# Kernel optimization log

Measured on AMD Instinct MI355X. Metric: run time of the kernel, lower is better.

## Reference

```python
import jax, jax.numpy as jnp
import numpy as np
from jax import lax

# dims
B, N, F = 128, 65536, 512


def setup_inputs() -> dict:
    key = jax.random.key(0)
    k1, k2 = jax.random.split(key)
    x = jax.random.normal(k1, (B, N), dtype=jnp.float32)          # dry audio
    logits = jax.random.normal(k2, (B, F, 5), dtype=jnp.float32)  # [bs, n_frames, 5]
    return {"x": x, "logits": logits}


def linear_interpolate_dim1(v, n_out):
    # v: [B, n_in, C] -> [B, n_out, C], linear interp with align_corners=True
    n_in = v.shape[1]
    pos = jnp.arange(n_out, dtype=jnp.float32) * ((n_in - 1) / (n_out - 1))
    i0 = jnp.clip(jnp.floor(pos).astype(jnp.int32), 0, n_in - 2)
    frac = (pos - i0.astype(jnp.float32))[None, :, None]
    return v[:, i0, :] * (1.0 - frac) + v[:, i0 + 1, :] * frac


def logits_to_a_coeff_triangle(a_logits):
    # stability-triangle parameterization: |a2| < 1 and |a1| < 1 + a2
    a1 = 2.0 * jnp.tanh(a_logits[..., 0])
    a1_abs = jnp.abs(a1)
    a2 = 0.5 * ((2.0 - a1_abs) * jnp.tanh(a_logits[..., 1]) + a1_abs)
    return jnp.stack([a1, a2], axis=-1)  # [B, F, 2]


def sample_wise_lpc2(x, a):
    # y[n] = x[n] - a1[n]*y[n-1] - a2[n]*y[n-2];  x: [B,N], a: [B,N,2]
    def step(carry, inp):
        y1, y2 = carry
        xn, a1, a2 = inp
        y = xn - a1 * y1 - a2 * y2
        return (y, y1), y
    z = jnp.zeros(x.shape[0], dtype=x.dtype)
    xs = (x.T, a[:, :, 0].T, a[:, :, 1].T)  # time-major
    _, ys = lax.scan(step, (z, z), xs)
    return ys.T


def time_varying_fir(x, b):
    # y[n] = b0[n]*x[n] + b1[n]*x[n-1] + b2[n]*x[n-2];  b: [B,N,3]
    xp = jnp.pad(x, ((0, 0), (2, 0)))
    return b[:, :, 0] * xp[:, 2:] + b[:, :, 1] * xp[:, 1:-1] + b[:, :, 2] * xp[:, :-2]


def reference(x, logits):
    n_samples = x.shape[1]
    # interp_logits=False: map a-logits to coeffs at frame rate, then interpolate
    a_coeff = logits_to_a_coeff_triangle(logits[..., :2])          # [B, F, 2]
    b_coeff = logits[..., 2:]                                      # [B, F, 3]
    a_coeff = linear_interpolate_dim1(a_coeff, n_samples)          # [B, N, 2]
    b_coeff = linear_interpolate_dim1(b_coeff, n_samples)          # [B, N, 3]
    y_a = sample_wise_lpc2(x, a_coeff)
    y_ab = time_varying_fir(y_a, b_coeff)
    return y_ab
```

## Files before the change

kernel.cpp:

```cpp
#include <hip/hip_runtime.h>
#include <hip/hip_bf16.h>

#define B_   128
#define N_   65536
#define F_   512
#define CS   64
#define CPR  (N_ / CS)
#define TPB  128
#define BPR  (CPR / TPB)
#define NBLK (B_ * BPR)
#define BLK_SAMP (TPB * CS)
#define KPOS ((float)(511.0 / 65535.0))
#define INVK ((float)(65535.0 / 511.0))
#define STRIDE 68
#define MAGIC 0x5A17F00Du

__device__ __forceinline__ float tanh_map1(float l) { return 2.0f * tanhf(l); }

__device__ __forceinline__ void chunk_geom(int n0, float& pos0, int& I, int& kc) {
    pos0 = (float)n0 * KPOS;
    I = min((int)pos0, F_ - 2);
    int k = (int)ceilf(((float)(I + 1) - pos0) * INVK);
    k = max(0, min(k, CS));
    if (k > 0 && (int)((float)(n0 + k - 1) * KPOS) > I) --k;
    else if (k < CS && (int)((float)(n0 + k) * KPOS) <= I) ++k;
    if ((int)pos0 > F_ - 2) k = CS;
    if (I == F_ - 2) {
        if ((float)n0 * KPOS >= (float)(F_ - 1)) k = CS;
    }
    kc = k;
}

__global__ __launch_bounds__(TPB, 2) void fused_lb(const float* __restrict__ x,
                                                   const float* __restrict__ logits,
                                                   float* __restrict__ agg,
                                                   unsigned int* __restrict__ flags,
                                                   float* __restrict__ out) {
    __shared__ __align__(16) float buf[TPB][STRIDE];
    __shared__ float sc[6][TPB];
    __shared__ float sbs[2];
    int tid = threadIdx.x;
    int gid = blockIdx.x;
    int gchunk0 = gid * TPB;

    const float4* xg = (const float4*)x + (size_t)gchunk0 * (CS / 4);
    #pragma unroll
    for (int it = 0; it < BLK_SAMP / 4 / TPB; ++it) {
        int i4 = it * TPB + tid;
        float4 v = xg[i4];
        *(float4*)&buf[i4 >> 4][(i4 & 15) * 4] = v;
    }
    __syncthreads();

    int t = gchunk0 + tid;
    int b = t >> 10;
    int c = t & (CPR - 1);
    int n0 = c * CS;

    float pos0; int I, kc;
    chunk_geom(n0, pos0, I, kc);
    int I2 = min(I + 2, F_ - 1);
    const float* Lg = logits + (size_t)b * F_ * 5;
    float a1A = tanh_map1(Lg[I * 5 + 0]);
    float a1B = tanh_map1(Lg[(I + 1) * 5 + 0]);
    float a1C = tanh_map1(Lg[I2 * 5 + 0]);
    float t1A = tanhf(Lg[I * 5 + 1]);
    float t1B = tanhf(Lg[(I + 1) * 5 + 1]);
    float t1C = tanhf(Lg[I2 * 5 + 1]);
    float a2A = 0.5f * ((2.0f - fabsf(a1A)) * t1A + fabsf(a1A));
    float a2B = 0.5f * ((2.0f - fabsf(a1B)) * t1B + fabsf(a1B));
    float a2C = 0.5f * ((2.0f - fabsf(a1C)) * t1C + fabsf(a1C));

    float If = (float)I;
    float C1  = fmaf(pos0 - If,        a1B - a1A, a1A), D1  = KPOS * (a1B - a1A);
    float C1b = fmaf(pos0 - If - 1.f,  a1C - a1B, a1B), D1b = KPOS * (a1C - a1B);
    float C2  = fmaf(pos0 - If,        a2B - a2A, a2A), D2  = KPOS * (a2B - a2A);
    float C2b = fmaf(pos0 - If - 1.f,  a2C - a2B, a2B), D2b = KPOS * (a2C - a2B);

    float A00 = 1.f, A01 = 0.f, A10 = 0.f, A11 = 1.f, v0 = 0.f, v1 = 0.f;
    #pragma unroll
    for (int j = 0; j < CS / 4; ++j) {
        float4 xv = *(const float4*)&buf[tid][j * 4];
        #pragma unroll
        for (int u = 0; u < 4; ++u) {
            int k = j * 4 + u;
            float xn = (&xv.x)[u];
            bool sB = (k >= kc);
            float kf = (float)k;
            float a1 = fmaf(kf, sB ? D1b : D1, sB ? C1b : C1);
            float a2 = fmaf(kf, sB ? D2b : D2, sB ? C2b : C2);
            float nA00 = fmaf(-a2, A10, -a1 * A00);
            float nA01 = fmaf(-a2, A11, -a1 * A01);
            float nv0  = fmaf(-a2, v1, fmaf(-a1, v0, xn));
            A10 = A00; A11 = A01; v1 = v0;
            A00 = nA00; A01 = nA01; v0 = nv0;
        }
    }

    for (int d = 1; d < TPB; d <<= 1) {
        sc[0][tid] = A00; sc[1][tid] = A01; sc[2][tid] = A10;
        sc[3][tid] = A11; sc[4][tid] = v0;  sc[5][tid] = v1;
        __syncthreads();
        if (tid >= d) {
            float f00 = sc[0][tid - d], f01 = sc[1][tid - d];
            float f10 = sc[2][tid - d], f11 = sc[3][tid - d];
            float fv0 = sc[4][tid - d], fv1 = sc[5][tid - d];
            float n00 = A00 * f00 + A01 * f10;
            float n01 = A00 * f01 + A01 * f11;
            float n10 = A10 * f00 + A11 * f10;
            float n11 = A10 * f01 + A11 * f11;
            float nv0 = A00 * fv0 + A01 * fv1 + v0;
            float nv1 = A10 * fv0 + A11 * fv1 + v1;
            A00 = n00; A01 = n01; A10 = n10; A11 = n11; v0 = nv0; v1 = nv1;
        }
        __syncthreads();
    }
    sc[0][tid] = A00; sc[1][tid] = A01; sc[2][tid] = A10;
    sc[3][tid] = A11; sc[4][tid] = v0;  sc[5][tid] = v1;
    __syncthreads();

    float L00, L01, L10, L11, Lv0, Lv1;
    if (tid == 0) { L00 = 1.f; L01 = 0.f; L10 = 0.f; L11 = 1.f; Lv0 = 0.f; Lv1 = 0.f; }
    else {
        L00 = sc[0][tid - 1]; L01 = sc[1][tid - 1];
        L10 = sc[2][tid - 1]; L11 = sc[3][tid - 1];
        Lv0 = sc[4][tid - 1]; Lv1 = sc[5][tid - 1];
    }
    __syncthreads();

    if (tid == TPB - 1) {
        float* T = agg + (size_t)gid * 6;
        __hip_atomic_store(&T[0], A00, __ATOMIC_RELAXED, __HIP_MEMORY_SCOPE_AGENT);
        __hip_atomic_store(&T[1], A01, __ATOMIC_RELAXED, __HIP_MEMORY_SCOPE_AGENT);
        __hip_atomic_store(&T[2], A10, __ATOMIC_RELAXED, __HIP_MEMORY_SCOPE_AGENT);
        __hip_atomic_store(&T[3], A11, __ATOMIC_RELAXED, __HIP_MEMORY_SCOPE_AGENT);
        __hip_atomic_store(&T[4], v0,  __ATOMIC_RELAXED, __HIP_MEMORY_SCOPE_AGENT);
        __hip_atomic_store(&T[5], v1,  __ATOMIC_RELAXED, __HIP_MEMORY_SCOPE_AGENT);
        __hip_atomic_store(&flags[gid], MAGIC, __ATOMIC_RELEASE, __HIP_MEMORY_SCOPE_AGENT);
    }

    int p0 = gid & ~(BPR - 1);
    int np = gid - p0;
    if (tid < np) {
        int p = p0 + tid;
        while (__hip_atomic_load(&flags[p], __ATOMIC_ACQUIRE, __HIP_MEMORY_SCOPE_AGENT)
               != MAGIC) {
            __builtin_amdgcn_s_sleep(1);
        }
        const float* T = agg + (size_t)p * 6;
        #pragma unroll
        for (int j = 0; j < 6; ++j)
            sc[j][tid] = __hip_atomic_load(&T[j], __ATOMIC_RELAXED, __HIP_MEMORY_SCOPE_AGENT);
    }
    __syncthreads();
    if (tid == 0) {
        float s0 = 0.f, s1 = 0.f;
        for (int p = 0; p < np; ++p) {
            float n0s = sc[0][p] * s0 + sc[1][p] * s1 + sc[4][p];
            float n1s = sc[2][p] * s0 + sc[3][p] * s1 + sc[5][p];
            s0 = n0s; s1 = n1s;
        }
        sbs[0] = s0; sbs[1] = s1;
    }

    float vA[5], vB[5], vC[5];
    vA[0] = a1A; vB[0] = a1B; vC[0] = a1C;
    vA[1] = a2A; vB[1] = a2B; vC[1] = a2C;
    #pragma unroll
    for (int j = 0; j < 3; ++j) {
        vA[2 + j] = Lg[I * 5 + 2 + j];
        vB[2 + j] = Lg[(I + 1) * 5 + 2 + j];
        vC[2 + j] = Lg[I2 * 5 + 2 + j];
    }
    float Cs[5], Ds[5], Csb[5], Dsb[5];
    #pragma unroll
    for (int j = 0; j < 5; ++j) {
        Cs[j]  = fmaf(pos0 - If,       vB[j] - vA[j], vA[j]);
        Ds[j]  = KPOS * (vB[j] - vA[j]);
        Csb[j] = fmaf(pos0 - If - 1.f, vC[j] - vB[j], vB[j]);
        Dsb[j] = KPOS * (vC[j] - vB[j]);
    }
    __syncthreads();

    float bs0 = sbs[0], bs1 = sbs[1];
    float s0v = L00 * bs0 + L01 * bs1 + Lv0;
    float s1v = L10 * bs0 + L11 * bs1 + Lv1;

    #pragma unroll
    for (int j = 0; j < CS / 4; ++j) {
        float4 xv = *(const float4*)&buf[tid][j * 4];
        float4 yv;
        #pragma unroll
        for (int u = 0; u < 4; ++u) {
            int k = j * 4 + u;
            float xn = (&xv.x)[u];
            bool sB = (k >= kc);
            float kf = (float)k;
            float a1 = fmaf(kf, sB ? Dsb[0] : Ds[0], sB ? Csb[0] : Cs[0]);
            float a2 = fmaf(kf, sB ? Dsb[1] : Ds[1], sB ? Csb[1] : Cs[1]);
            float b0 = fmaf(kf, sB ? Dsb[2] : Ds[2], sB ? Csb[2] : Cs[2]);
            float b1 = fmaf(kf, sB ? Dsb[3] : Ds[3], sB ? Csb[3] : Cs[3]);
            float b2 = fmaf(kf, sB ? Dsb[4] : Ds[4], sB ? Csb[4] : Cs[4]);
            float y = fmaf(-a2, s1v, fmaf(-a1, s0v, xn));
            (&yv.x)[u] = fmaf(b2, s1v, fmaf(b1, s0v, b0 * y));
            s1v = s0v; s0v = y;
        }
        *(float4*)&buf[tid][j * 4] = yv;
    }
    __syncthreads();

    float4* og = (float4*)out + (size_t)gchunk0 * (CS / 4);
    #pragma unroll
    for (int it = 0; it < BLK_SAMP / 4 / TPB; ++it) {
        int i4 = it * TPB + tid;
        og[i4] = *(float4*)&buf[i4 >> 4][(i4 & 15) * 4];
    }
}

extern "C" void kernel_launch(void* const* d_in, const int* in_sizes, int n_in,
                              void* d_out, int out_size, void* d_ws, size_t ws_size,
                              hipStream_t stream) {
    const float* x      = (const float*)d_in[0];
    const float* logits = (const float*)d_in[1];
    float* out = (float*)d_out;
    float* ws  = (float*)d_ws;

    float* agg = ws;
    unsigned int* flags = (unsigned int*)(ws + 6 * NBLK);

    fused_lb<<<NBLK, TPB, 0, stream>>>(x, logits, agg, flags, out);
}
```

Before: 116.8 us.

## Process one full row per 1024-thread block with wave-shuffle scan

Each block now handles an entire batch row (1024 threads x 64-sample chunks), which removes the cross-block decoupled look-back through global flags and workspace. The intra-block scan uses wavefront shuffles plus a small serial combine over 16 wave aggregates, and the LDS staging of x and out is replaced by direct strided float4 global loads and stores, with x read twice. Only 128 blocks are launched, so the grid may underfill the GPU's CUs, and per-thread 256-byte strided accesses lose coalescing.

Result: slower. 135.8 us (+16.2%).

```diff
diff --git a/kernel.cpp b/kernel.cpp
--- a/kernel.cpp
+++ b/kernel.cpp
@@ -6,14 +6,10 @@
 #define F_   512
 #define CS   64
 #define CPR  (N_ / CS)
-#define TPB  128
-#define BPR  (CPR / TPB)
-#define NBLK (B_ * BPR)
-#define BLK_SAMP (TPB * CS)
+#define TPB  1024
+#define NWAVE (TPB / 64)
 #define KPOS ((float)(511.0 / 65535.0))
 #define INVK ((float)(65535.0 / 511.0))
-#define STRIDE 68
-#define MAGIC 0x5A17F00Du
 
 __device__ __forceinline__ float tanh_map1(float l) { return 2.0f * tanhf(l); }
 
@@ -31,36 +27,22 @@
     kc = k;
 }
 
-__global__ __launch_bounds__(TPB, 2) void fused_lb(const float* __restrict__ x,
-                                                   const float* __restrict__ logits,
-                                                   float* __restrict__ agg,
-                                                   unsigned int* __restrict__ flags,
-                                                   float* __restrict__ out) {
-    __shared__ __align__(16) float buf[TPB][STRIDE];
-    __shared__ float sc[6][TPB];
-    __shared__ float sbs[2];
-    int tid = threadIdx.x;
-    int gid = blockIdx.x;
-    int gchunk0 = gid * TPB;
-
-    const float4* xg = (const float4*)x + (size_t)gchunk0 * (CS / 4);
-    #pragma unroll
-    for (int it = 0; it < BLK_SAMP / 4 / TPB; ++it) {
-        int i4 = it * TPB + tid;
-        float4 v = xg[i4];
-        *(float4*)&buf[i4 >> 4][(i4 & 15) * 4] = v;
-    }
-    __syncthreads();
-
-    int t = gchunk0 + tid;
-    int b = t >> 10;
-    int c = t & (CPR - 1);
-    int n0 = c * CS;
+__global__ __launch_bounds__(TPB, 4) void fused_row(const float* __restrict__ x,
+                                                    const float* __restrict__ logits,
+                                                    float* __restrict__ out) {
+    __shared__ float wagg[NWAVE][6];
+    __shared__ float wpv[NWAVE][2];
+    int tid  = threadIdx.x;
+    int b    = blockIdx.x;
+    int lane = tid & 63;
+    int wid  = tid >> 6;
+    int n0   = tid * CS;
 
     float pos0; int I, kc;
     chunk_geom(n0, pos0, I, kc);
     int I2 = min(I + 2, F_ - 1);
     const float* Lg = logits + (size_t)b * F_ * 5;
+
     float a1A = tanh_map1(Lg[I * 5 + 0]);
     float a1B = tanh_map1(Lg[(I + 1) * 5 + 0]);
     float a1C = tanh_map1(Lg[I2 * 5 + 0]);
@@ -77,10 +59,11 @@
     float C2  = fmaf(pos0 - If,        a2B - a2A, a2A), D2  = KPOS * (a2B - a2A);
     float C2b = fmaf(pos0 - If - 1.f,  a2C - a2B, a2B), D2b = KPOS * (a2C - a2B);
 
+    const float4* xp = (const float4*)x + ((size_t)b * N_ + n0) / 4;
     float A00 = 1.f, A01 = 0.f, A10 = 0.f, A11 = 1.f, v0 = 0.f, v1 = 0.f;
     #pragma unroll
     for (int j = 0; j < CS / 4; ++j) {
-        float4 xv = *(const float4*)&buf[tid][j * 4];
+        float4 xv = xp[j];
         #pragma unroll
         for (int u = 0; u < 4; ++u) {
             int k = j * 4 + u;
@@ -97,14 +80,15 @@
         }
     }
 
-    for (int d = 1; d < TPB; d <<= 1) {
-        sc[0][tid] = A00; sc[1][tid] = A01; sc[2][tid] = A10;
-        sc[3][tid] = A11; sc[4][tid] = v0;  sc[5][tid] = v1;
-        __syncthreads();
-        if (tid >= d) {
-            float f00 = sc[0][tid - d], f01 = sc[1][tid - d];
-            float f10 = sc[2][tid - d], f11 = sc[3][tid - d];
-            float fv0 = sc[4][tid - d], fv1 = sc[5][tid - d];
+    #pragma unroll
+    for (int d = 1; d < 64; d <<= 1) {
+        float f00 = __shfl_up(A00, d);
+        float f01 = __shfl_up(A01, d);
+        float f10 = __shfl_up(A10, d);
+        float f11 = __shfl_up(A11, d);
+        float fv0 = __shfl_up(v0, d);
+        float fv1 = __shfl_up(v1, d);
+        if (lane >= d) {
             float n00 = A00 * f00 + A01 * f10;
             float n01 = A00 * f01 + A01 * f11;
             float n10 = A10 * f00 + A11 * f10;
@@ -113,54 +97,27 @@
             float nv1 = A10 * fv0 + A11 * fv1 + v1;
             A00 = n00; A01 = n01; A10 = n10; A11 = n11; v0 = nv0; v1 = nv1;
         }
-        __syncthreads();
     }
-    sc[0][tid] = A00; sc[1][tid] = A01; sc[2][tid] = A10;
-    sc[3][tid] = A11; sc[4][tid] = v0;  sc[5][tid] = v1;
-    __syncthreads();
 
-    float L00, L01, L10, L11, Lv0, Lv1;
-    if (tid == 0) { L00 = 1.f; L01 = 0.f; L10 = 0.f; L11 = 1.f; Lv0 = 0.f; Lv1 = 0.f; }
-    else {
-        L00 = sc[0][tid - 1]; L01 = sc[1][tid - 1];
-        L10 = sc[2][tid - 1]; L11 = sc[3][tid - 1];
-        Lv0 = sc[4][tid - 1]; Lv1 = sc[5][tid - 1];
+    float e00 = __shfl_up(A00, 1), e01 = __shfl_up(A01, 1);
+    float e10 = __shfl_up(A10, 1), e11 = __shfl_up(A11, 1);
+    float ev0 = __shfl_up(v0, 1),  ev1 = __shfl_up(v1, 1);
+    if (lane == 0) { e00 = 1.f; e01 = 0.f; e10 = 0.f; e11 = 1.f; ev0 = 0.f; ev1 = 0.f; }
+
+    if (lane == 63) {
+        wagg[wid][0] = A00; wagg[wid][1] = A01; wagg[wid][2] = A10;
+        wagg[wid][3] = A11; wagg[wid][4] = v0;  wagg[wid][5] = v1;
     }
     __syncthreads();
 
-    if (tid == TPB - 1) {
-        float* T = agg + (size_t)gid * 6;
-        __hip_atomic_store(&T[0], A00, __ATOMIC_RELAXED, __HIP_MEMORY_SCOPE_AGENT);
-        __hip_atomic_store(&T[1], A01, __ATOMIC_RELAXED, __HIP_MEMORY_SCOPE_AGENT);
-        __hip_atomic_store(&T[2], A10, __ATOMIC_RELAXED, __HIP_MEMORY_SCOPE_AGENT);
-        __hip_atomic_store(&T[3], A11, __ATOMIC_RELAXED, __HIP_MEMORY_SCOPE_AGENT);
-        __hip_atomic_store(&T[4], v0,  __ATOMIC_RELAXED, __HIP_MEMORY_SCOPE_AGENT);
-        __hip_atomic_store(&T[5], v1,  __ATOMIC_RELAXED, __HIP_MEMORY_SCOPE_AGENT);
-        __hip_atomic_store(&flags[gid], MAGIC, __ATOMIC_RELEASE, __HIP_MEMORY_SCOPE_AGENT);
-    }
-
-    int p0 = gid & ~(BPR - 1);
-    int np = gid - p0;
-    if (tid < np) {
-        int p = p0 + tid;
-        while (__hip_atomic_load(&flags[p], __ATOMIC_ACQUIRE, __HIP_MEMORY_SCOPE_AGENT)
-               != MAGIC) {
-            __builtin_amdgcn_s_sleep(1);
-        }
-        const float* T = agg + (size_t)p * 6;
-        #pragma unroll
-        for (int j = 0; j < 6; ++j)
-            sc[j][tid] = __hip_atomic_load(&T[j], __ATOMIC_RELAXED, __HIP_MEMORY_SCOPE_AGENT);
-    }
-    __syncthreads();
-    if (tid == 0) {
+    if (lane == 0) {
         float s0 = 0.f, s1 = 0.f;
-        for (int p = 0; p < np; ++p) {
-            float n0s = sc[0][p] * s0 + sc[1][p] * s1 + sc[4][p];
-            float n1s = sc[2][p] * s0 + sc[3][p] * s1 + sc[5][p];
+        for (int p = 0; p < wid; ++p) {
+            float n0s = wagg[p][0] * s0 + wagg[p][1] * s1 + wagg[p][4];
+            float n1s = wagg[p][2] * s0 + wagg[p][3] * s1 + wagg[p][5];
             s0 = n0s; s1 = n1s;
         }
-        sbs[0] = s0; sbs[1] = s1;
+        wpv[wid][0] = s0; wpv[wid][1] = s1;
     }
 
     float vA[5], vB[5], vC[5];
@@ -182,13 +139,14 @@
     }
     __syncthreads();
 
-    float bs0 = sbs[0], bs1 = sbs[1];
-    float s0v = L00 * bs0 + L01 * bs1 + Lv0;
-    float s1v = L10 * bs0 + L11 * bs1 + Lv1;
+    float bs0 = wpv[wid][0], bs1 = wpv[wid][1];
+    float s0v = e00 * bs0 + e01 * bs1 + ev0;
+    float s1v = e10 * bs0 + e11 * bs1 + ev1;
 
+    float4* op = (float4*)out + ((size_t)b * N_ + n0) / 4;
     #pragma unroll
     for (int j = 0; j < CS / 4; ++j) {
-        float4 xv = *(const float4*)&buf[tid][j * 4];
+        float4 xv = xp[j];
         float4 yv;
         #pragma unroll
         for (int u = 0; u < 4; ++u) {
@@ -205,15 +163,7 @@
             (&yv.x)[u] = fmaf(b2, s1v, fmaf(b1, s0v, b0 * y));
             s1v = s0v; s0v = y;
         }
-        *(float4*)&buf[tid][j * 4] = yv;
-    }
-    __syncthreads();
-
-    float4* og = (float4*)out + (size_t)gchunk0 * (CS / 4);
-    #pragma unroll
-    for (int it = 0; it < BLK_SAMP / 4 / TPB; ++it) {
-        int i4 = it * TPB + tid;
-        og[i4] = *(float4*)&buf[i4 >> 4][(i4 & 15) * 4];
+        op[j] = yv;
     }
 }
 
@@ -223,10 +173,7 @@
     const float* x      = (const float*)d_in[0];
     const float* logits = (const float*)d_in[1];
     float* out = (float*)d_out;
-    float* ws  = (float*)d_ws;
+    (void)d_ws; (void)ws_size;
 
-    float* agg = ws;
-    unsigned int* flags = (unsigned int*)(ws + 6 * NBLK);
-
-    fused_lb<<<NBLK, TPB, 0, stream>>>(x, logits, agg, flags, out);
+    fused_row<<<B_, TPB, 0, stream>>>(x, logits, out);
 }
```
